# Optimization experiments

Measured on AMD Instinct MI355X. Metric: run time of the kernel, lower is better.

Reference implementation:

```python
import jax, jax.numpy as jnp
import numpy as np

D_MODEL = 1024
HEADS = 16
HEAD_DIM = D_MODEL // HEADS


def setup_inputs() -> dict:
    key = jax.random.key(0)
    k1, k2 = jax.random.split(key)
    x = jax.random.normal(k1, (2, 2048, D_MODEL), dtype=jnp.float32)
    # nn.Linear(d_model, 3*d_model, bias=False): weight shape [3*d_model, d_model]
    W_qkv = jax.random.normal(k2, (3 * D_MODEL, D_MODEL), dtype=jnp.float32) * (D_MODEL ** -0.5)
    return {"x": x, "W_qkv": W_qkv}


def reference(x, W_qkv):
    b, t, c = x.shape
    qkv = jnp.einsum('btc,fc->btf', x, W_qkv)  # [b, t, 3c]
    q, k, v = jnp.split(qkv, 3, axis=-1)
    # [b, heads, t, head_dim]
    q = q.reshape(b, t, HEADS, HEAD_DIM).transpose(0, 2, 1, 3)
    k = k.reshape(b, t, HEADS, HEAD_DIM).transpose(0, 2, 1, 3)
    v = v.reshape(b, t, HEADS, HEAD_DIM).transpose(0, 2, 1, 3)
    scores = jnp.einsum('bhqd,bhkd->bhqk', q, k) * (HEAD_DIM ** -0.5)
    causal = jnp.tril(jnp.ones((t, t), dtype=bool))  # [t, t]
    scores = jnp.where(causal[None, None, :, :], scores, -jnp.inf)
    weights = jax.nn.softmax(scores, axis=-1)
    out = jnp.einsum('bhqk,bhkd->bhqd', weights, v)
    return out.transpose(0, 2, 1, 3).reshape(b, t, c)
```

## Files before the change

kernel.cpp:

```cpp
#include <hip/hip_runtime.h>
#include <hip/hip_bf16.h>
#include <stdint.h>

#define D_MODEL 1024
#define TOKENS  2048
#define HEADS   16
#define HDIM    64
#define NQKV    3072
#define MROWS   4096
#define SCALE   0.18033688011112042f

typedef __attribute__((ext_vector_type(4)))  float f32x4;
typedef __attribute__((ext_vector_type(16))) float f32x16;
typedef __attribute__((ext_vector_type(8)))  short bf16x8;

__device__ __forceinline__ unsigned short f2bf(float f) {
  union { float f; unsigned u; } v; v.f = f;
  unsigned u = v.u + 0x7FFFu + ((v.u >> 16) & 1u);
  return (unsigned short)(u >> 16);
}
__device__ __forceinline__ float bf2f(unsigned short b) {
  union { unsigned u; float f; } v; v.u = ((unsigned)b) << 16;
  return v.f;
}
__device__ __forceinline__ unsigned cvt_pk_bf16(float lo, float hi) {
  unsigned r;
  asm("v_cvt_pk_bf16_f32 %0, %1, %2" : "=v"(r) : "v"(lo), "v"(hi));
  return r;
}
__device__ __forceinline__ float xchg32(float v) {
  return __shfl_xor(v, 32);
}
__device__ __forceinline__ bf16x8 pfrag8(const float* g) {
  union { uint4 u; bf16x8 v; } r;
  r.u.x = cvt_pk_bf16(g[0], g[1]);
  r.u.y = cvt_pk_bf16(g[2], g[3]);
  r.u.z = cvt_pk_bf16(g[4], g[5]);
  r.u.w = cvt_pk_bf16(g[6], g[7]);
  return r.v;
}
__device__ __forceinline__ float max32t(const f32x16& a, const f32x16& b) {
  float t[16];
#pragma unroll
  for (int r = 0; r < 16; ++r) t[r] = fmaxf(a[r], b[r]);
#pragma unroll
  for (int s = 8; s > 0; s >>= 1)
#pragma unroll
    for (int r = 0; r < s; ++r) t[r] = fmaxf(t[r], t[r + s]);
  return t[0];
}
__device__ __forceinline__ float sum32t(const float* a, const float* b) {
  float t[16];
#pragma unroll
  for (int r = 0; r < 16; ++r) t[r] = a[r] + b[r];
#pragma unroll
  for (int s = 8; s > 0; s >>= 1)
#pragma unroll
    for (int r = 0; r < s; ++r) t[r] = t[r] + t[r + s];
  return t[0];
}

#define GLOAD16(g, l)                                                          \
  __builtin_amdgcn_global_load_lds(                                            \
      (const __attribute__((address_space(1))) unsigned int*)(g),              \
      (__attribute__((address_space(3))) unsigned int*)(l), 16, 0, 0)

__global__ __launch_bounds__(256) void cvt_bf16(const float* __restrict__ X,
                                                const float* __restrict__ W,
                                                unsigned short* __restrict__ Xb,
                                                unsigned short* __restrict__ Wb) {
  const size_t NX = (size_t)MROWS * D_MODEL;
  size_t i = ((size_t)blockIdx.x * 256 + threadIdx.x) * 8;
  const float* src; unsigned short* dst; size_t off;
  if (i < NX) { src = X; dst = Xb; off = i; }
  else        { src = W; dst = Wb; off = i - NX; }
  float4 a = ((const float4*)(src + off))[0];
  float4 b = ((const float4*)(src + off))[1];
  union { unsigned short s[8]; uint4 v; } u;
  u.s[0] = f2bf(a.x); u.s[1] = f2bf(a.y); u.s[2] = f2bf(a.z); u.s[3] = f2bf(a.w);
  u.s[4] = f2bf(b.x); u.s[5] = f2bf(b.y); u.s[6] = f2bf(b.z); u.s[7] = f2bf(b.w);
  *(uint4*)(dst + off) = u.v;
}

__global__ __launch_bounds__(512, 1) void gemm8(const unsigned short* __restrict__ A,
                                                const unsigned short* __restrict__ B,
                                                unsigned short* __restrict__ C) {
  __shared__ unsigned short sA[2][2][128][64];
  __shared__ unsigned short sB[2][2][128][64];

  const int tid  = threadIdx.x;
  const int lane = tid & 63;
  const int wave = tid >> 6;
  const int wr   = wave >> 2;
  const int wc   = wave & 3;
  const int l15  = lane & 15;
  const int lg   = lane >> 4;

  const int bm = blockIdx.x;
  const int bn = blockIdx.y;

  f32x4 acc[8][4];
#pragma unroll
  for (int i = 0; i < 8; ++i)
#pragma unroll
    for (int j = 0; j < 4; ++j)
#pragma unroll
      for (int r = 0; r < 4; ++r) acc[i][j][r] = 0.f;

  const int srow = tid >> 3;
  const int scb  = (tid & 7) * 16;
  const int ssce = (scb ^ ((srow & 4) << 3)) >> 1;

  const unsigned short* Ag = A + (size_t)(bm * 256) * D_MODEL;
  const unsigned short* Bg = B + (size_t)(bn * 256) * D_MODEL;

#define STG_A(buf, hf, t)                                                      \
  { GLOAD16(Ag + (size_t)((hf) * 128 + srow) * D_MODEL + (t) * 64 + ssce,      \
            (char*)&sA[buf][hf][0][0] + srow * 128 + scb);                     \
    GLOAD16(Ag + (size_t)((hf) * 128 + 64 + srow) * D_MODEL + (t) * 64 + ssce, \
            (char*)&sA[buf][hf][0][0] + 8192 + srow * 128 + scb); }
#define STG_B(buf, hf, t)                                                      \
  { GLOAD16(Bg + (size_t)((hf) * 128 + srow) * D_MODEL + (t) * 64 + ssce,      \
            (char*)&sB[buf][hf][0][0] + srow * 128 + scb);                     \
    GLOAD16(Bg + (size_t)((hf) * 128 + 64 + srow) * D_MODEL + (t) * 64 + ssce, \
            (char*)&sB[buf][hf][0][0] + 8192 + srow * 128 + scb); }

  const char* aBse[2] = { (const char*)&sA[0][wr][0][0], (const char*)&sA[1][wr][0][0] };
  const char* bBse[2] = { (const char*)&sB[0][wc >> 1][0][0], (const char*)&sB[1][wc >> 1][0][0] };
  const int swzl = (l15 & 4) << 3;
  const int cbs0 = (lg * 16) ^ swzl;
  const int cbs1 = (64 + lg * 16) ^ swzl;
  const int arow = l15 * 128;
  const int brow = ((wc & 1) * 64 + l15) * 128;

#define DO_PHASE(qm, qn, buf, STAGE_STMT, DO_VM)                               \
  {                                                                            \
    bf16x8 a_[4][2], b_[2][2];                                                 \
    _Pragma("unroll")                                                          \
    for (int i = 0; i < 4; ++i) {                                              \
      a_[i][0] = *(const bf16x8*)(aBse[buf] + ((qm)*4 + i) * 2048 + arow + cbs0); \
      a_[i][1] = *(const bf16x8*)(aBse[buf] + ((qm)*4 + i) * 2048 + arow + cbs1); \
    }                                                                          \
    _Pragma("unroll")                                                          \
    for (int n = 0; n < 2; ++n) {                                              \
      b_[n][0] = *(const bf16x8*)(bBse[buf] + ((qn)*2 + n) * 2048 + brow + cbs0); \
      b_[n][1] = *(const bf16x8*)(bBse[buf] + ((qn)*2 + n) * 2048 + brow + cbs1); \
    }                                                                          \
    STAGE_STMT;                                                                \
    if (DO_VM) asm volatile("s_waitcnt vmcnt(2)" ::: "memory");                \
    __builtin_amdgcn_s_barrier();                                              \
    asm volatile("s_waitcnt lgkmcnt(0)" ::: "memory");                         \
    __builtin_amdgcn_sched_barrier(0);                                         \
    __builtin_amdgcn_s_setprio(1);                                             \
    _Pragma("unroll")                                                          \
    for (int ks = 0; ks < 2; ++ks)                                             \
      _Pragma("unroll")                                                        \
      for (int i = 0; i < 4; ++i)                                              \
        _Pragma("unroll")                                                      \
        for (int n = 0; n < 2; ++n)                                            \
          acc[(qm)*4 + i][(qn)*2 + n] = __builtin_amdgcn_mfma_f32_16x16x32_bf16( \
              a_[i][ks], b_[n][ks], acc[(qm)*4 + i][(qn)*2 + n], 0, 0, 0);     \
    __builtin_amdgcn_s_setprio(0);                                             \
    __builtin_amdgcn_s_barrier();                                              \
  }

  STG_A(0, 0, 0);
  STG_B(0, 0, 0);
  STG_A(0, 1, 0);
  STG_B(0, 1, 0);
  STG_B(1, 0, 1);
  asm volatile("s_waitcnt vmcnt(2)" ::: "memory");
  __builtin_amdgcn_s_barrier();

#pragma unroll 1
  for (int j = 0; j < 8; ++j) {
    const int t1 = 2 * j + 1;
    const int t2 = 2 * j + 2;
    const int t3 = 2 * j + 3;
    DO_PHASE(0, 0, 0, { STG_A(1, 0, t1); }, 0);
    DO_PHASE(1, 0, 0, { STG_A(1, 1, t1); }, 0);
    DO_PHASE(0, 1, 0, { STG_B(1, 1, t1); }, 0);
    DO_PHASE(1, 1, 0, { if (t2 < 16) STG_B(0, 0, t2); }, 1);
    DO_PHASE(0, 0, 1, { if (t2 < 16) STG_A(0, 0, t2); }, 0);
    DO_PHASE(1, 0, 1, { if (t2 < 16) STG_A(0, 1, t2); }, 0);
    DO_PHASE(0, 1, 1, { if (t2 < 16) STG_B(0, 1, t2); }, 0);
    DO_PHASE(1, 1, 1, { if (t3 < 16) STG_B(1, 0, t3); }, 1);
  }

  const int orow0 = bm * 256 + wr * 128 + lg * 4;
  const int ocol0 = bn * 256 + wc * 64 + l15;
#pragma unroll
  for (int mi = 0; mi < 8; ++mi)
#pragma unroll
    for (int ni = 0; ni < 4; ++ni)
#pragma unroll
      for (int r = 0; r < 4; ++r)
        C[(size_t)(orow0 + mi * 16 + r) * NQKV + ocol0 + ni * 16] = f2bf(acc[mi][ni][r]);
#undef STG_A
#undef STG_B
#undef DO_PHASE
}

__global__ __launch_bounds__(256) void qkv_gemm(const float* __restrict__ X,
                                                const float* __restrict__ W,
                                                unsigned short* __restrict__ QKV) {
  __shared__ unsigned short sA[128 * 32];
  __shared__ unsigned short sB[128 * 32];
  const int tid  = threadIdx.x;
  const int lane = tid & 63;
  const int wave = tid >> 6;
  const int wr = wave >> 1, wc = wave & 1;
  const int row0 = blockIdx.x * 128;
  const int col0 = blockIdx.y * 128;

  f32x4 acc[4][4];
#pragma unroll
  for (int i = 0; i < 4; ++i)
#pragma unroll
    for (int j = 0; j < 4; ++j)
#pragma unroll
      for (int r = 0; r < 4; ++r) acc[i][j][r] = 0.f;

  const int srow = tid >> 1;
  const int scol = (tid & 1) * 16;
  union U16 { unsigned short s[8]; uint4 v; };

#pragma unroll 1
  for (int k0 = 0; k0 < D_MODEL; k0 += 32) {
    {
      const float* ga = X + (size_t)(row0 + srow) * D_MODEL + k0 + scol;
      const float* gb = W + (size_t)(col0 + srow) * D_MODEL + k0 + scol;
      float va[16], vb[16];
#pragma unroll
      for (int i = 0; i < 4; ++i) {
        float4 t = ((const float4*)ga)[i];
        va[4*i+0] = t.x; va[4*i+1] = t.y; va[4*i+2] = t.z; va[4*i+3] = t.w;
        float4 u = ((const float4*)gb)[i];
        vb[4*i+0] = u.x; vb[4*i+1] = u.y; vb[4*i+2] = u.z; vb[4*i+3] = u.w;
      }
      U16 ua0, ua1, ub0, ub1;
#pragma unroll
      for (int e = 0; e < 8; ++e) {
        ua0.s[e] = f2bf(va[e]);   ua1.s[e] = f2bf(va[8 + e]);
        ub0.s[e] = f2bf(vb[e]);   ub1.s[e] = f2bf(vb[8 + e]);
      }
      *(uint4*)&sA[srow * 32 + scol + 0] = ua0.v;
      *(uint4*)&sA[srow * 32 + scol + 8] = ua1.v;
      *(uint4*)&sB[srow * 32 + scol + 0] = ub0.v;
      *(uint4*)&sB[srow * 32 + scol + 8] = ub1.v;
    }
    __syncthreads();

    const int lrow = lane & 15;
    const int lk   = (lane >> 4) * 8;
    bf16x8 av[4], bv[4];
#pragma unroll
    for (int i = 0; i < 4; ++i)
      av[i] = *(const bf16x8*)&sA[(wr * 64 + i * 16 + lrow) * 32 + lk];
#pragma unroll
    for (int j = 0; j < 4; ++j)
      bv[j] = *(const bf16x8*)&sB[(wc * 64 + j * 16 + lrow) * 32 + lk];
#pragma unroll
    for (int i = 0; i < 4; ++i)
#pragma unroll
      for (int j = 0; j < 4; ++j)
        acc[i][j] = __builtin_amdgcn_mfma_f32_16x16x32_bf16(av[i], bv[j], acc[i][j], 0, 0, 0);
    __syncthreads();
  }

  const int orow = row0 + wr * 64 + (lane >> 4) * 4;
  const int ocol = col0 + wc * 64 + (lane & 15);
#pragma unroll
  for (int i = 0; i < 4; ++i)
#pragma unroll
    for (int j = 0; j < 4; ++j)
#pragma unroll
      for (int r = 0; r < 4; ++r)
        QKV[(size_t)(orow + i * 16 + r) * NQKV + ocol + j * 16] = f2bf(acc[i][j][r]);
}

__global__ __launch_bounds__(256, 2) void attn9(const unsigned short* __restrict__ QKV,
                                                float* __restrict__ Out) {
  __shared__ unsigned short sK [2][2][64 * 64];
  __shared__ unsigned short sVt[2][2][64 * 64];

  const int tid  = threadIdx.x;
  const int lane = tid & 63;
  const int wave = tid >> 6;
  const int l31  = lane & 31;
  const int hi   = lane >> 5;

  const int x = blockIdx.x;
  int bh, u;
  if (x < 256) { bh = x & 31; u = x >> 5; }
  else         { const int x2 = x - 256; bh = x2 & 31; u = 15 - (x2 >> 5); }

  const int b = bh >> 4, h = bh & 15;
  const int q0w  = u * 128 + wave * 32;
  const int qcol = q0w + l31;

  const unsigned short* Qbase = QKV + (size_t)(b * TOKENS) * NQKV + h * HDIM;
  const unsigned short* Kbase = Qbase + D_MODEL;
  const unsigned short* Vbase = Kbase + D_MODEL;

  bf16x8 qf[4];
  {
    const unsigned short* qrow = Qbase + (size_t)qcol * NQKV + hi * 8;
    union { unsigned short us[8]; bf16x8 v; ushort4 q[2]; } t;
#pragma unroll
    for (int dk = 0; dk < 4; ++dk) {
      t.q[0] = ((const ushort4*)(qrow + dk * 16))[0];
      t.q[1] = ((const ushort4*)(qrow + dk * 16))[1];
#pragma unroll
      for (int e = 0; e < 8; ++e) t.us[e] = f2bf(bf2f(t.us[e]) * SCALE);
      qf[dk] = t.v;
    }
  }

  f32x16 o0, o1;
#pragma unroll
  for (int r = 0; r < 16; ++r) { o0[r] = 0.f; o1[r] = 0.f; }
  float m = -1e30f, l = 0.f;

  const int vk0 = (tid & 15) * 4;
  const int vd0 = (tid >> 4) * 4;
  ushort4 va0, va1, va2, va3, vb0, vb1, vb2, vb3;

  const int lane16 = lane * 16;

#define KGLOAD(kt, buf, s)                                                     \
  {                                                                            \
    _Pragma("unroll")                                                          \
    for (int g = 0; g < 2; ++g) {                                              \
      const int base = g * 4096 + wave * 1024;                                 \
      const int d = base + lane16;                                             \
      const int row = d >> 7;                                                  \
      const int grow = (row & 51) | ((row & 4) << 1) | ((row & 8) >> 1);       \
      const int cb = (d & 127) ^ ((row & 7) << 4);                             \
      GLOAD16(Kbase + (size_t)((kt) * 64 + grow) * NQKV + (cb >> 1),           \
              (char*)&sK[buf][s][0] + base + lane16);                          \
    }                                                                          \
  }

#define VLOAD2(pp)                                                             \
  {                                                                            \
    const unsigned short* vsA = Vbase + (size_t)((2*(pp)) * 64 + vk0) * NQKV + vd0;   \
    va0 = *(const ushort4*)(vsA);                                              \
    va1 = *(const ushort4*)(vsA + NQKV);                                       \
    va2 = *(const ushort4*)(vsA + 2 * NQKV);                                   \
    va3 = *(const ushort4*)(vsA + 3 * NQKV);                                   \
    const unsigned short* vsB = Vbase + (size_t)((2*(pp)+1) * 64 + vk0) * NQKV + vd0; \
    vb0 = *(const ushort4*)(vsB);                                              \
    vb1 = *(const ushort4*)(vsB + NQKV);                                       \
    vb2 = *(const ushort4*)(vsB + 2 * NQKV);                                   \
    vb3 = *(const ushort4*)(vsB + 3 * NQKV);                                   \
  }

#define VWRITE1(buf, s, t0, t1, t2, t3)                                        \
  {                                                                            \
    ushort4 c0, c1, c2, c3;                                                    \
    c0.x = t0.x; c0.y = t1.x; c0.z = t2.x; c0.w = t3.x;                        \
    c1.x = t0.y; c1.y = t1.y; c1.z = t2.y; c1.w = t3.y;                        \
    c2.x = t0.z; c2.y = t1.z; c2.z = t2.z; c2.w = t3.z;                        \
    c3.x = t0.w; c3.y = t1.w; c3.z = t2.w; c3.w = t3.w;                        \
    char* dV = (char*)&sVt[buf][s][0];                                         \
    _Pragma("unroll")                                                          \
    for (int e = 0; e < 4; ++e) {                                              \
      const int dim = vd0 + e;                                                 \
      const int o2 = (dim * 128 + vk0 * 2) ^ ((dim & 7) << 4);                 \
      ushort4 cc = (e == 0) ? c0 : (e == 1) ? c1 : (e == 2) ? c2 : c3;         \
      *(ushort4*)(dV + o2) = cc;                                               \
    }                                                                          \
  }

#define QKT(cK, rowbase, st)                                                   \
  {                                                                            \
    _Pragma("unroll")                                                          \
    for (int dk = 0; dk < 4; ++dk) {                                           \
      const int row = (rowbase);                                               \
      bf16x8 kf = *(const bf16x8*)((cK) + ((row * 128 + hi * 16 + dk * 32) ^ ((row & 7) << 4))); \
      st = __builtin_amdgcn_mfma_f32_32x32x16_bf16(kf, qf[dk], st, 0, 0, 0);   \
    }                                                                          \
  }

#define PV4(cV, bpX, bpY, koff)                                                \
  {                                                                            \
    const int r0 = l31, r1 = l31 + 32;                                         \
    bf16x8 vf;                                                                 \
    vf = *(const bf16x8*)((cV) + ((r0 * 128 + hi * 16 + (koff)) ^ ((r0 & 7) << 4)));      \
    o0 = __builtin_amdgcn_mfma_f32_32x32x16_bf16(vf, bpX, o0, 0, 0, 0);        \
    vf = *(const bf16x8*)((cV) + ((r1 * 128 + hi * 16 + (koff)) ^ ((r1 & 7) << 4)));      \
    o1 = __builtin_amdgcn_mfma_f32_32x32x16_bf16(vf, bpX, o1, 0, 0, 0);        \
    vf = *(const bf16x8*)((cV) + ((r0 * 128 + hi * 16 + (koff) + 32) ^ ((r0 & 7) << 4))); \
    o0 = __builtin_amdgcn_mfma_f32_32x32x16_bf16(vf, bpY, o0, 0, 0, 0);        \
    vf = *(const bf16x8*)((cV) + ((r1 * 128 + hi * 16 + (koff) + 32) ^ ((r1 & 7) << 4))); \
    o1 = __builtin_amdgcn_mfma_f32_32x32x16_bf16(vf, bpY, o1, 0, 0, 0);        \
  }

  KGLOAD(0, 0, 0);
  KGLOAD(1, 0, 1);
  VLOAD2(0);
  VWRITE1(0, 0, va0, va1, va2, va3);
  VWRITE1(0, 1, vb0, vb1, vb2, vb3);
  __syncthreads();

#pragma unroll 1
  for (int p = 0; p < u; ++p) {
    const int cur = p & 1;
    KGLOAD(2 * (p + 1),     cur ^ 1, 0);
    KGLOAD(2 * (p + 1) + 1, cur ^ 1, 1);
    VLOAD2(p + 1);

    const char* cKA = (const char*)&sK[cur][0][0];
    const char* cKB = (const char*)&sK[cur][1][0];
    const char* cVA = (const char*)&sVt[cur][0][0];
    const char* cVB = (const char*)&sVt[cur][1][0];

    f32x16 sA0, sA1, sB0, sB1;
#pragma unroll
    for (int r = 0; r < 16; ++r) { sA0[r] = 0.f; sA1[r] = 0.f; sB0[r] = 0.f; sB1[r] = 0.f; }

    QKT(cKA, l31,      sA0);
    QKT(cKA, l31 + 32, sA1);
    QKT(cKB, l31,      sB0);
    QKT(cKB, l31 + 32, sB1);

    {
      float mx = max32t(sA0, sA1);
      mx = fmaxf(mx, xchg32(mx));
      if (!__all(mx - m <= 8.f)) {
        const float mnew = fmaxf(m, mx);
        const float corr = exp2f(m - mnew);
        m = mnew;
        l *= corr;
#pragma unroll
        for (int r = 0; r < 16; ++r) { o0[r] *= corr; o1[r] *= corr; }
      }
      float pA0[16], pA1[16];
#pragma unroll
      for (int r = 0; r < 16; ++r) { pA0[r] = exp2f(sA0[r] - m); pA1[r] = exp2f(sA1[r] - m); }
      float ps = sum32t(pA0, pA1);
      ps += xchg32(ps);
      l += ps;
      bf16x8 a0 = pfrag8(&pA0[0]), a1 = pfrag8(&pA0[8]);
      bf16x8 a2 = pfrag8(&pA1[0]), a3 = pfrag8(&pA1[8]);
      PV4(cVA, a0, a1, 0);
      PV4(cVA, a2, a3, 64);
    }

    {
      float mx = max32t(sB0, sB1);
      mx = fmaxf(mx, xchg32(mx));
      if (!__all(mx - m <= 8.f)) {
        const float mnew = fmaxf(m, mx);
        const float corr = exp2f(m - mnew);
        m = mnew;
        l *= corr;
#pragma unroll
        for (int r = 0; r < 16; ++r) { o0[r] *= corr; o1[r] *= corr; }
      }
      float pB0[16], pB1[16];
#pragma unroll
      for (int r = 0; r < 16; ++r) { pB0[r] = exp2f(sB0[r] - m); pB1[r] = exp2f(sB1[r] - m); }
      float ps = sum32t(pB0, pB1);
      ps += xchg32(ps);
      l += ps;
      bf16x8 b0 = pfrag8(&pB0[0]), b1 = pfrag8(&pB0[8]);
      bf16x8 b2 = pfrag8(&pB1[0]), b3 = pfrag8(&pB1[8]);
      PV4(cVB, b0, b1, 0);
      PV4(cVB, b2, b3, 64);
    }

    VWRITE1(cur ^ 1, 0, va0, va1, va2, va3);
    VWRITE1(cur ^ 1, 1, vb0, vb1, vb2, vb3);
    __syncthreads();
  }

  {
    const int cur = u & 1;
    const char* cK[2] = { (const char*)&sK[cur][0][0], (const char*)&sK[cur][1][0] };
    const char* cV[2] = { (const char*)&sVt[cur][0][0], (const char*)&sVt[cur][1][0] };
    const int nsub = (wave >= 2) ? 2 : 1;
#pragma unroll 1
    for (int s = 0; s < nsub; ++s) {
      const int kbase = u * 128 + s * 64;
      const bool diag  = (wave >= 2) ? (s == 1) : true;
      const bool do_hi = diag ? ((wave & 1) == 1) : true;

      f32x16 st0, st1;
#pragma unroll
      for (int r = 0; r < 16; ++r) { st0[r] = 0.f; st1[r] = 0.f; }

      QKT(cK[s], l31, st0);
      if (do_hi) QKT(cK[s], l31 + 32, st1);

      if (diag) {
#pragma unroll
        for (int r = 0; r < 16; ++r) {
          const int key0 = kbase + (r & 7) + ((r & 8) << 1) + 8 * hi;
          if (key0 > qcol) st0[r] = -1e30f;
          if (do_hi && key0 + 32 > qcol) st1[r] = -1e30f;
        }
      }

      float mx = do_hi ? max32t(st0, st1) : max32t(st0, st0);
      mx = fmaxf(mx, xchg32(mx));

      if (!__all(mx - m <= 8.f)) {
        const float mnew = fmaxf(m, mx);
        const float corr = exp2f(m - mnew);
        m = mnew;
        l *= corr;
#pragma unroll
        for (int r = 0; r < 16; ++r) { o0[r] *= corr; o1[r] *= corr; }
      }

      float p0[16], p1[16];
#pragma unroll
      for (int r = 0; r < 16; ++r) p0[r] = exp2f(st0[r] - m);
      float ps;
      if (do_hi) {
#pragma unroll
        for (int r = 0; r < 16; ++r) p1[r] = exp2f(st1[r] - m);
        ps = sum32t(p0, p1);
      } else {
        float z[16];
#pragma unroll
        for (int r = 0; r < 16; ++r) z[r] = 0.f;
        ps = sum32t(p0, z);
      }
      ps += xchg32(ps);
      l += ps;

      bf16x8 c0 = pfrag8(&p0[0]), c1 = pfrag8(&p0[8]);
      PV4(cV[s], c0, c1, 0);
      if (do_hi) {
        bf16x8 c2 = pfrag8(&p1[0]), c3 = pfrag8(&p1[8]);
        PV4(cV[s], c2, c3, 64);
      }
    }
  }

  {
    const float inv = 1.f / l;
    float* orow = Out + (size_t)(b * TOKENS + qcol) * D_MODEL + h * HDIM;
#pragma unroll
    for (int g = 0; g < 4; ++g) {
      float4 w0, w1;
      w0.x = o0[4*g+0] * inv; w0.y = o0[4*g+1] * inv;
      w0.z = o0[4*g+2] * inv; w0.w = o0[4*g+3] * inv;
      w1.x = o1[4*g+0] * inv; w1.y = o1[4*g+1] * inv;
      w1.z = o1[4*g+2] * inv; w1.w = o1[4*g+3] * inv;
      *(float4*)(orow + 8 * g + 4 * hi)      = w0;
      *(float4*)(orow + 8 * g + 4 * hi + 32) = w1;
    }
  }
}

extern "C" void kernel_launch(void* const* d_in, const int* in_sizes, int n_in,
                              void* d_out, int out_size, void* d_ws, size_t ws_size,
                              hipStream_t stream) {
  const float* X = (const float*)d_in[0];
  const float* W = (const float*)d_in[1];
  float* Out = (float*)d_out;
  unsigned short* QKV = (unsigned short*)d_ws;

  const size_t QKV_E = (size_t)MROWS * NQKV;
  const size_t XB_E  = (size_t)MROWS * D_MODEL;
  const size_t WB_E  = (size_t)NQKV * D_MODEL;
  const size_t need_bf16 = (QKV_E + XB_E + WB_E) * 2;

  if (ws_size >= need_bf16) {
    unsigned short* Xb = QKV + QKV_E;
    unsigned short* Wb = Xb + XB_E;
    cvt_bf16<<<(XB_E + WB_E) / (256 * 8), 256, 0, stream>>>(X, W, Xb, Wb);
    gemm8<<<dim3(MROWS / 256, NQKV / 256), 512, 0, stream>>>(Xb, Wb, QKV);
  } else {
    qkv_gemm<<<dim3(MROWS / 128, NQKV / 128), 256, 0, stream>>>(X, W, QKV);
  }

  attn9<<<512, 256, 0, stream>>>(QKV, Out);
}
```

Before: 110.1 us.

## Split causal attention into key chunks with a merge kernel; widen GEMM LDS swizzle

Result: slower. 150.9 us (+37.1%).

```diff
diff --git a/kernel.cpp b/kernel.cpp
--- a/kernel.cpp
+++ b/kernel.cpp
@@ -109,7 +109,7 @@
 
   const int srow = tid >> 3;
   const int scb  = (tid & 7) * 16;
-  const int ssce = (scb ^ ((srow & 4) << 3)) >> 1;
+  const int ssce = (scb ^ ((srow & 7) << 4)) >> 1;
 
   const unsigned short* Ag = A + (size_t)(bm * 256) * D_MODEL;
   const unsigned short* Bg = B + (size_t)(bn * 256) * D_MODEL;
@@ -127,7 +127,7 @@
 
   const char* aBse[2] = { (const char*)&sA[0][wr][0][0], (const char*)&sA[1][wr][0][0] };
   const char* bBse[2] = { (const char*)&sB[0][wc >> 1][0][0], (const char*)&sB[1][wc >> 1][0][0] };
-  const int swzl = (l15 & 4) << 3;
+  const int swzl = (l15 & 7) << 4;
   const int cbs0 = (lg * 16) ^ swzl;
   const int cbs1 = (64 + lg * 16) ^ swzl;
   const int arow = l15 * 128;
@@ -279,6 +279,310 @@
         QKV[(size_t)(orow + i * 16 + r) * NQKV + ocol + j * 16] = f2bf(acc[i][j][r]);
 }
 
+__global__ __launch_bounds__(128, 4) void attn_ch(const unsigned short* __restrict__ QKV,
+                                                  float* __restrict__ Out,
+                                                  unsigned short* __restrict__ Opart,
+                                                  float* __restrict__ ML) {
+  __shared__ unsigned short sK [2][64 * 64];
+  __shared__ unsigned short sVt[2][64 * 64];
+
+  const int tid  = threadIdx.x;
+  const int lane = tid & 63;
+  const int wave = tid >> 6;
+  const int l31  = lane & 31;
+  const int hi   = lane >> 5;
+
+  const int e  = blockIdx.x;
+  int qt, c, nc;
+  if (e < 8)       { qt = e;                    c = 0;      nc = 1; }
+  else if (e < 24) { int u = e - 8;  qt = 8  + (u >> 1); c = u & 1;  nc = 2; }
+  else if (e < 48) { int u = e - 24; qt = 16 + u / 3;    c = u % 3;  nc = 3; }
+  else             { int u = e - 48; qt = 24 + (u >> 2); c = u & 3;  nc = 4; }
+
+  const int bh = blockIdx.y;
+  const int b = bh >> 4, h = bh & 15;
+
+  const int T0 = 8 * c;
+  const int T1 = min(8 * c + 8, qt + 1);
+  const int count = T1 - T0;
+  const int np  = count >> 1;
+  const int odd = count & 1;
+  const int nsteps = np + odd;
+
+  const unsigned short* Qbase = QKV + (size_t)(b * TOKENS) * NQKV + h * HDIM;
+  const unsigned short* Kbase = Qbase + D_MODEL;
+  const unsigned short* Vbase = Kbase + D_MODEL;
+
+  const int qcol = qt * 64 + wave * 32 + l31;
+
+  bf16x8 qf[4];
+  {
+    const unsigned short* qrow = Qbase + (size_t)qcol * NQKV + hi * 8;
+    union { unsigned short us[8]; bf16x8 v; ushort4 q[2]; } t;
+#pragma unroll
+    for (int dk = 0; dk < 4; ++dk) {
+      t.q[0] = ((const ushort4*)(qrow + dk * 16))[0];
+      t.q[1] = ((const ushort4*)(qrow + dk * 16))[1];
+#pragma unroll
+      for (int ee = 0; ee < 8; ++ee) t.us[ee] = f2bf(bf2f(t.us[ee]) * SCALE);
+      qf[dk] = t.v;
+    }
+  }
+
+  f32x16 o0, o1;
+#pragma unroll
+  for (int r = 0; r < 16; ++r) { o0[r] = 0.f; o1[r] = 0.f; }
+  float m = -1e30f, l = 0.f;
+
+  const int lane16 = lane * 16;
+  const int vk0 = (tid & 15) * 4;
+  const int vd0 = (tid >> 4) * 8;
+
+  union VU { uint4 v; unsigned short us[8]; };
+  VU va0, va1, va2, va3, vb0, vb1, vb2, vb3;
+
+#define KGLOAD1(sb, kt)                                                        \
+  {                                                                            \
+    _Pragma("unroll")                                                          \
+    for (int g = 0; g < 4; ++g) {                                              \
+      const int d = g * 2048 + wave * 1024 + lane16;                           \
+      const int row = d >> 7;                                                  \
+      const int grow = (row & 51) | ((row & 4) << 1) | ((row & 8) >> 1);       \
+      const int cb = (d & 127) ^ ((row & 7) << 4);                             \
+      GLOAD16(Kbase + (size_t)((kt) * 64 + grow) * NQKV + (cb >> 1),           \
+              (char*)&sK[sb][0] + d);                                          \
+    }                                                                          \
+  }
+
+#define VLOAD1(kt, r0, r1, r2, r3)                                             \
+  {                                                                            \
+    const unsigned short* vs = Vbase + (size_t)((kt) * 64 + vk0) * NQKV + vd0; \
+    r0.v = *(const uint4*)(vs);                                                \
+    r1.v = *(const uint4*)(vs + NQKV);                                         \
+    r2.v = *(const uint4*)(vs + 2 * NQKV);                                     \
+    r3.v = *(const uint4*)(vs + 3 * NQKV);                                     \
+  }
+
+#define VWRITE8(sb, r0, r1, r2, r3)                                            \
+  {                                                                            \
+    char* dV = (char*)&sVt[sb][0];                                             \
+    _Pragma("unroll")                                                          \
+    for (int ee = 0; ee < 8; ++ee) {                                           \
+      const int dim = vd0 + ee;                                                \
+      uint2 w;                                                                 \
+      w.x = (unsigned)r0.us[ee] | ((unsigned)r1.us[ee] << 16);                 \
+      w.y = (unsigned)r2.us[ee] | ((unsigned)r3.us[ee] << 16);                 \
+      *(uint2*)(dV + ((dim * 128 + vk0 * 2) ^ ((dim & 7) << 4))) = w;          \
+    }                                                                          \
+  }
+
+#define QKT(cK, rowbase, st)                                                   \
+  {                                                                            \
+    _Pragma("unroll")                                                          \
+    for (int dk = 0; dk < 4; ++dk) {                                           \
+      const int row = (rowbase);                                               \
+      bf16x8 kf = *(const bf16x8*)((cK) + ((row * 128 + hi * 16 + dk * 32) ^ ((row & 7) << 4))); \
+      st = __builtin_amdgcn_mfma_f32_32x32x16_bf16(kf, qf[dk], st, 0, 0, 0);   \
+    }                                                                          \
+  }
+
+#define PV4(cV, bpX, bpY, koff)                                                \
+  {                                                                            \
+    const int r0_ = l31, r1_ = l31 + 32;                                       \
+    bf16x8 vf;                                                                 \
+    vf = *(const bf16x8*)((cV) + ((r0_ * 128 + hi * 16 + (koff)) ^ ((r0_ & 7) << 4)));      \
+    o0 = __builtin_amdgcn_mfma_f32_32x32x16_bf16(vf, bpX, o0, 0, 0, 0);        \
+    vf = *(const bf16x8*)((cV) + ((r1_ * 128 + hi * 16 + (koff)) ^ ((r1_ & 7) << 4)));      \
+    o1 = __builtin_amdgcn_mfma_f32_32x32x16_bf16(vf, bpX, o1, 0, 0, 0);        \
+    vf = *(const bf16x8*)((cV) + ((r0_ * 128 + hi * 16 + (koff) + 32) ^ ((r0_ & 7) << 4))); \
+    o0 = __builtin_amdgcn_mfma_f32_32x32x16_bf16(vf, bpY, o0, 0, 0, 0);        \
+    vf = *(const bf16x8*)((cV) + ((r1_ * 128 + hi * 16 + (koff) + 32) ^ ((r1_ & 7) << 4))); \
+    o1 = __builtin_amdgcn_mfma_f32_32x32x16_bf16(vf, bpY, o1, 0, 0, 0);        \
+  }
+
+#define SUBSTEP(cK, cV, tile, diagF)                                           \
+  {                                                                            \
+    const bool diag  = (diagF);                                                \
+    const bool do_hi = !(diag && wave == 0);                                   \
+    f32x16 st0, st1;                                                           \
+    _Pragma("unroll")                                                          \
+    for (int r = 0; r < 16; ++r) { st0[r] = 0.f; st1[r] = 0.f; }               \
+    QKT(cK, l31, st0);                                                         \
+    if (do_hi) QKT(cK, l31 + 32, st1);                                         \
+    if (diag) {                                                                \
+      const int kbase = (tile) * 64;                                           \
+      _Pragma("unroll")                                                        \
+      for (int r = 0; r < 16; ++r) {                                           \
+        const int key0 = kbase + (r & 7) + ((r & 8) << 1) + 8 * hi;            \
+        if (key0 > qcol) st0[r] = -1e30f;                                      \
+        if (do_hi && key0 + 32 > qcol) st1[r] = -1e30f;                        \
+      }                                                                        \
+    }                                                                          \
+    float mx = do_hi ? max32t(st0, st1) : max32t(st0, st0);                    \
+    mx = fmaxf(mx, xchg32(mx));                                                \
+    if (!__all(mx - m <= 8.f)) {                                               \
+      const float mnew = fmaxf(m, mx);                                         \
+      const float corr = exp2f(m - mnew);                                      \
+      m = mnew;                                                                \
+      l *= corr;                                                               \
+      _Pragma("unroll")                                                        \
+      for (int r = 0; r < 16; ++r) { o0[r] *= corr; o1[r] *= corr; }           \
+    }                                                                          \
+    float p0[16], p1[16];                                                      \
+    _Pragma("unroll")                                                          \
+    for (int r = 0; r < 16; ++r) p0[r] = exp2f(st0[r] - m);                    \
+    float ps;                                                                  \
+    if (do_hi) {                                                               \
+      _Pragma("unroll")                                                        \
+      for (int r = 0; r < 16; ++r) p1[r] = exp2f(st1[r] - m);                  \
+      ps = sum32t(p0, p1);                                                     \
+    } else {                                                                   \
+      float z[16];                                                             \
+      _Pragma("unroll")                                                        \
+      for (int r = 0; r < 16; ++r) z[r] = 0.f;                                 \
+      ps = sum32t(p0, z);                                                      \
+    }                                                                          \
+    ps += xchg32(ps);                                                          \
+    l += ps;                                                                   \
+    bf16x8 f0 = pfrag8(&p0[0]), f1 = pfrag8(&p0[8]);                           \
+    PV4(cV, f0, f1, 0);                                                        \
+    if (do_hi) {                                                               \
+      bf16x8 f2 = pfrag8(&p1[0]), f3 = pfrag8(&p1[8]);                         \
+      PV4(cV, f2, f3, 64);                                                     \
+    }                                                                          \
+  }
+
+  {
+    const int ta = T0;
+    const int tb = min(T0 + 1, T1 - 1);
+    VLOAD1(ta, va0, va1, va2, va3);
+    VLOAD1(tb, vb0, vb1, vb2, vb3);
+  }
+
+#pragma unroll 1
+  for (int i = 0; i < nsteps; ++i) {
+    const int ta = T0 + 2 * i;
+    const int tb = min(ta + 1, T1 - 1);
+    const bool is_pair = (i < np);
+
+    __syncthreads();
+    KGLOAD1(0, ta);
+    KGLOAD1(1, tb);
+    VWRITE8(0, va0, va1, va2, va3);
+    VWRITE8(1, vb0, vb1, vb2, vb3);
+    const bool more = (i + 1 < nsteps);
+    if (more) {
+      const int na = T0 + 2 * (i + 1);
+      const int nb = min(na + 1, T1 - 1);
+      VLOAD1(na, va0, va1, va2, va3);
+      VLOAD1(nb, vb0, vb1, vb2, vb3);
+    }
+    if (more) asm volatile("s_waitcnt vmcnt(8)" ::: "memory");
+    else      asm volatile("s_waitcnt vmcnt(0)" ::: "memory");
+    asm volatile("s_waitcnt lgkmcnt(0)" ::: "memory");
+    __builtin_amdgcn_s_barrier();
+
+    SUBSTEP((const char*)&sK[0][0], (const char*)&sVt[0][0], ta, ta == qt);
+    if (is_pair)
+      SUBSTEP((const char*)&sK[1][0], (const char*)&sVt[1][0], tb, tb == qt);
+  }
+
+  if (nc == 1) {
+    const float inv = 1.f / l;
+    float* orow = Out + (size_t)(b * TOKENS + qcol) * D_MODEL + h * HDIM;
+#pragma unroll
+    for (int g = 0; g < 4; ++g) {
+      float4 w0, w1;
+      w0.x = o0[4*g+0] * inv; w0.y = o0[4*g+1] * inv;
+      w0.z = o0[4*g+2] * inv; w0.w = o0[4*g+3] * inv;
+      w1.x = o1[4*g+0] * inv; w1.y = o1[4*g+1] * inv;
+      w1.z = o1[4*g+2] * inv; w1.w = o1[4*g+3] * inv;
+      *(float4*)(orow + 8 * g + 4 * hi)      = w0;
+      *(float4*)(orow + 8 * g + 4 * hi + 32) = w1;
+    }
+  } else {
+    const int qloc = wave * 32 + l31;
+    unsigned short* ob = Opart + ((size_t)(bh * 80 + e)) * 4096 + qloc * 64;
+#pragma unroll
+    for (int g = 0; g < 4; ++g) {
+      uint2 w0, w1;
+      w0.x = cvt_pk_bf16(o0[4*g+0], o0[4*g+1]);
+      w0.y = cvt_pk_bf16(o0[4*g+2], o0[4*g+3]);
+      w1.x = cvt_pk_bf16(o1[4*g+0], o1[4*g+1]);
+      w1.y = cvt_pk_bf16(o1[4*g+2], o1[4*g+3]);
+      *(uint2*)(ob + 8 * g + 4 * hi)      = w0;
+      *(uint2*)(ob + 8 * g + 4 * hi + 32) = w1;
+    }
+    if (hi == 0) {
+      float2 t2; t2.x = m; t2.y = l;
+      ((float2*)ML)[((size_t)(bh * 80 + e)) * 64 + qloc] = t2;
+    }
+  }
+#undef KGLOAD1
+#undef VLOAD1
+#undef VWRITE8
+#undef QKT
+#undef PV4
+#undef SUBSTEP
+}
+
+__global__ __launch_bounds__(256) void merge_split(const unsigned short* __restrict__ Opart,
+                                                   const float* __restrict__ ML,
+                                                   float* __restrict__ Out) {
+  const int qt = 8 + blockIdx.x;
+  const int bh = blockIdx.y;
+  const int b = bh >> 4, h = bh & 15;
+  int nc, slot0;
+  if (qt < 16)      { nc = 2; slot0 = 8  + (qt - 8)  * 2; }
+  else if (qt < 24) { nc = 3; slot0 = 24 + (qt - 16) * 3; }
+  else              { nc = 4; slot0 = 48 + (qt - 24) * 4; }
+
+  const int q  = threadIdx.x >> 2;
+  const int d0 = (threadIdx.x & 3) * 16;
+
+  float m[4], l[4];
+  float M = -1e30f;
+#pragma unroll 1
+  for (int si = 0; si < nc; ++si) {
+    float2 t = ((const float2*)ML)[((size_t)(bh * 80 + slot0 + si)) * 64 + q];
+    m[si] = t.x; l[si] = t.y;
+    M = fmaxf(M, t.x);
+  }
+  float L = 0.f, w[4];
+#pragma unroll 1
+  for (int si = 0; si < nc; ++si) { w[si] = exp2f(m[si] - M); L += l[si] * w[si]; }
+  const float invL = 1.f / L;
+
+  float acc[16];
+#pragma unroll
+  for (int i = 0; i < 16; ++i) acc[i] = 0.f;
+#pragma unroll 1
+  for (int si = 0; si < nc; ++si) {
+    const unsigned short* ob = Opart + ((size_t)(bh * 80 + slot0 + si)) * 4096 + q * 64 + d0;
+    ushort4 u0 = ((const ushort4*)ob)[0];
+    ushort4 u1 = ((const ushort4*)ob)[1];
+    ushort4 u2 = ((const ushort4*)ob)[2];
+    ushort4 u3 = ((const ushort4*)ob)[3];
+    const float ws = w[si];
+    acc[0]  += bf2f(u0.x) * ws; acc[1]  += bf2f(u0.y) * ws;
+    acc[2]  += bf2f(u0.z) * ws; acc[3]  += bf2f(u0.w) * ws;
+    acc[4]  += bf2f(u1.x) * ws; acc[5]  += bf2f(u1.y) * ws;
+    acc[6]  += bf2f(u1.z) * ws; acc[7]  += bf2f(u1.w) * ws;
+    acc[8]  += bf2f(u2.x) * ws; acc[9]  += bf2f(u2.y) * ws;
+    acc[10] += bf2f(u2.z) * ws; acc[11] += bf2f(u2.w) * ws;
+    acc[12] += bf2f(u3.x) * ws; acc[13] += bf2f(u3.y) * ws;
+    acc[14] += bf2f(u3.z) * ws; acc[15] += bf2f(u3.w) * ws;
+  }
+  float* orow = Out + (size_t)(b * TOKENS + qt * 64 + q) * D_MODEL + h * HDIM + d0;
+#pragma unroll
+  for (int i = 0; i < 4; ++i) {
+    float4 o;
+    o.x = acc[4*i+0] * invL; o.y = acc[4*i+1] * invL;
+    o.z = acc[4*i+2] * invL; o.w = acc[4*i+3] * invL;
+    ((float4*)orow)[i] = o;
+  }
+}
+
 __global__ __launch_bounds__(256, 2) void attn9(const unsigned short* __restrict__ QKV,
                                                 float* __restrict__ Out) {
   __shared__ unsigned short sK [2][2][64 * 64];
@@ -565,10 +869,14 @@
   float* Out = (float*)d_out;
   unsigned short* QKV = (unsigned short*)d_ws;
 
-  const size_t QKV_E = (size_t)MROWS * NQKV;
-  const size_t XB_E  = (size_t)MROWS * D_MODEL;
-  const size_t WB_E  = (size_t)NQKV * D_MODEL;
-  const size_t need_bf16 = (QKV_E + XB_E + WB_E) * 2;
+  const size_t QKV_E   = (size_t)MROWS * NQKV;
+  const size_t XB_E    = (size_t)MROWS * D_MODEL;
+  const size_t WB_E    = (size_t)NQKV * D_MODEL;
+  const size_t OPART_E = (size_t)32 * 80 * 4096;
+  const size_t ML_B    = (size_t)32 * 80 * 64 * 2 * sizeof(float);
+
+  const size_t need_bf16  = (QKV_E + XB_E + WB_E) * 2;
+  const size_t need_split = need_bf16 + OPART_E * 2 + ML_B;
 
   if (ws_size >= need_bf16) {
     unsigned short* Xb = QKV + QKV_E;
@@ -579,5 +887,12 @@
     qkv_gemm<<<dim3(MROWS / 128, NQKV / 128), 256, 0, stream>>>(X, W, QKV);
   }
 
-  attn9<<<512, 256, 0, stream>>>(QKV, Out);
-}
+  if (ws_size >= need_split) {
+    unsigned short* Opart = QKV + QKV_E + XB_E + WB_E;
+    float* ML = (float*)(Opart + OPART_E);
+    attn_ch<<<dim3(80, 2 * HEADS), 128, 0, stream>>>(QKV, Out, Opart, ML);
+    merge_split<<<dim3(24, 2 * HEADS), 256, 0, stream>>>(Opart, ML, Out);
+  } else {
+    attn9<<<512, 256, 0, stream>>>(QKV, Out);
+  }
+}
```
